# Optimization experiments

Hardware: AMD Instinct MI355X
Metric: run time of the kernel (lower is better)

Reference implementation:

```python
import jax, jax.numpy as jnp
import numpy as np

B, N, D = 16, 1024, 1152
H = 16; DH = D // H
GH = GW = 32; SY = SX = 2
WS = SY * SX                      # tokens per window
NW = (GH // SY) * (GW // SX)      # 256 windows (one dst each)
NS = NW * (WS - 1)                # 768 src tokens
NUM_PRUNE = int(N * 0.5)          # 512
NOISE_ALPHA = 0.1
SIM_BETA = 1.0


def setup_inputs() -> dict:
    key = jax.random.key(0)
    ks = jax.random.split(key, 8)
    rn = lambda k, s: jax.random.normal(k, s, jnp.float32) * 0.02
    return dict(
        x=jax.random.normal(ks[0], (B, N, D), jnp.float32),
        noise=jax.random.uniform(ks[1], (B, NW, WS), jnp.float32),
        ln1_g=jnp.ones((D,), jnp.float32), ln1_b=jnp.zeros((D,), jnp.float32),
        ln2_g=jnp.ones((D,), jnp.float32), ln2_b=jnp.zeros((D,), jnp.float32),
        w_qkv=rn(ks[2], (D, 3 * D)), b_qkv=jnp.zeros((3 * D,), jnp.float32),
        w_proj=rn(ks[3], (D, D)), b_proj=jnp.zeros((D,), jnp.float32),
        w_fc1=rn(ks[4], (D, 4 * D)), b_fc1=jnp.zeros((4 * D,), jnp.float32),
        w_fc2=rn(ks[5], (4 * D, D)), b_fc2=jnp.zeros((D,), jnp.float32),
    )


def _ln(x, g, b):
    mu = x.mean(-1, keepdims=True)
    var = ((x - mu) ** 2).mean(-1, keepdims=True)
    return (x - mu) * jax.lax.rsqrt(var + 1e-6) * g + b


def _dit_block(x, ln1_g, ln1_b, ln2_g, ln2_b, w_qkv, b_qkv, w_proj, b_proj,
               w_fc1, b_fc1, w_fc2, b_fc2):
    Bq, T, _ = x.shape
    y = _ln(x, ln1_g, ln1_b)
    q, k, v = jnp.split(y @ w_qkv + b_qkv, 3, axis=-1)
    hd = lambda t: t.reshape(Bq, T, H, DH).transpose(0, 2, 1, 3)  # [B,H,T,DH]
    q, k, v = hd(q), hd(k), hd(v)
    att = jax.nn.softmax(jnp.einsum('bhqd,bhkd->bhqk', q, k) * (1.0 / np.sqrt(DH)), axis=-1)
    o = jnp.einsum('bhqk,bhkd->bhqd', att, v).transpose(0, 2, 1, 3).reshape(Bq, T, D)
    x = x + o @ w_proj + b_proj
    y = _ln(x, ln2_g, ln2_b)
    return x + jax.nn.gelu(y @ w_fc1 + b_fc1) @ w_fc2 + b_fc2


def _sito_indices(x, noise):
    # SiTo seed (dst) selection + similarity-based prune index computation.
    xn = x / (jnp.linalg.norm(x, axis=-1, keepdims=True) + 1e-6)  # cosine feats
    grid = jnp.arange(N).reshape(GH, GW)
    win = grid.reshape(GH // SY, SY, GW // SX, SX).transpose(0, 2, 1, 3).reshape(NW, WS)
    xw = xn[:, win]                                   # [B,NW,WS,D]
    mean = xw.mean(2, keepdims=True)
    score = SIM_BETA * (xw * mean).sum(-1) + NOISE_ALPHA * noise  # [B,NW,WS]
    dst_local = jnp.argmax(score, axis=-1)            # [B,NW]
    winb = jnp.broadcast_to(win, (B, NW, WS))
    dst_idx = jnp.take_along_axis(winb, dst_local[..., None], -1)[..., 0]  # [B,NW]
    local = jnp.arange(WS)[None, None]
    keymat = jnp.where(local != dst_local[..., None], local, WS)
    src_local = jnp.sort(keymat, -1)[..., : WS - 1]   # non-dst locals, in order
    src_idx = jnp.take_along_axis(winb, src_local, -1).reshape(B, NS)
    a = jnp.take_along_axis(xn, src_idx[..., None], 1)      # [B,NS,D]
    bf = jnp.take_along_axis(xn, dst_idx[..., None], 1)     # [B,NW,D]
    sim = jnp.einsum('bsd,bnd->bsn', a, bf)                 # [B,NS,NW]
    best = jnp.argmax(sim, -1)                              # most-similar dst
    order = jnp.argsort(-jnp.max(sim, -1), axis=-1)
    pruned_pos = order[:, :NUM_PRUNE]
    kept_pos = order[:, NUM_PRUNE:]
    src_kept = jnp.take_along_axis(src_idx, kept_pos, 1)
    src_pruned = jnp.take_along_axis(src_idx, pruned_pos, 1)
    pruned_best = jnp.take_along_axis(best, pruned_pos, 1)
    return dst_idx, src_kept, src_pruned, pruned_best


def reference(x, noise, ln1_g, ln1_b, ln2_g, ln2_b, w_qkv, b_qkv, w_proj, b_proj,
              w_fc1, b_fc1, w_fc2, b_fc2):
    dst_idx, src_kept, src_pruned, pruned_best = _sito_indices(x, noise)
    keep_idx = jnp.concatenate([dst_idx, src_kept], axis=1)          # [B,Nk]
    xk = jnp.take_along_axis(x, keep_idx[..., None], 1)              # prune_fn
    out = _dit_block(xk, ln1_g, ln1_b, ln2_g, ln2_b, w_qkv, b_qkv,
                     w_proj, b_proj, w_fc1, b_fc1, w_fc2, b_fc2)

    def recover_one(o, di, sk, sp, pb):  # recover_fn: scatter + copy-from-dst
        out_dst, out_src = o[:NW], o[NW:]
        full = jnp.zeros((N, D), o.dtype)
        full = full.at[di].set(out_dst)
        full = full.at[sk].set(out_src)
        return full.at[sp].set(out_dst[pb])

    return jax.vmap(recover_one)(out, dst_idx, src_kept, src_pruned, pruned_best)
```

## Files before the change

kernel.cpp:

```cpp
#include <hip/hip_runtime.h>
#include <hip/hip_bf16.h>

namespace {

constexpr int Dd = 1152;

typedef __attribute__((ext_vector_type(8))) short bf16x8;
typedef __attribute__((ext_vector_type(4))) float f32x4;

__device__ __forceinline__ void gload_lds16(const void* g, void* l) {
  __builtin_amdgcn_global_load_lds(
      (const __attribute__((address_space(1))) void*)g,
      (__attribute__((address_space(3))) void*)l, 16, 0, 0);
}

__device__ __forceinline__ float gelu_f(float x) {
  float x3 = x * x * x;
  float z2 = 1.5957691216057308f * (x + 0.044715f * x3);
  float e = __expf(fminf(z2, 30.0f));
  return x * e / (e + 1.0f);
}

__global__ __launch_bounds__(256) void normwin_kernel(const float* __restrict__ x,
    const float* __restrict__ noise, float* __restrict__ inv,
    __hip_bfloat16* __restrict__ xnh, __hip_bfloat16* __restrict__ xnl,
    int* __restrict__ dsti, int* __restrict__ srci) {
  const int gidx = blockIdx.x;
  const int b = gidx >> 8, w = gidx & 255;
  const int wy = w >> 4, wx = w & 15;
  const int t0 = wy * 64 + wx * 2;
  const int wid = threadIdx.x >> 6, lane = threadIdx.x & 63;
  const int tok = t0 + (wid >> 1) * 32 + (wid & 1);
  const int row = (b << 10) + tok;

  const float2* xr = (const float2*)(x + (size_t)row * Dd);
  float2 v[9];
  float s = 0.f;
  #pragma unroll
  for (int e = 0; e < 9; ++e) {
    v[e] = xr[lane + 64 * e];
    s += v[e].x * v[e].x + v[e].y * v[e].y;
  }
  #pragma unroll
  for (int m = 1; m < 64; m <<= 1) s += __shfl_xor(s, m);
  float iv = 1.0f / (sqrtf(s) + 1e-6f);
  if (lane == 0) inv[row] = iv;

  __shared__ float2 xns[4][576];
  ushort2* ph = (ushort2*)(xnh + (size_t)row * Dd);
  ushort2* pl = (ushort2*)(xnl + (size_t)row * Dd);
  #pragma unroll
  for (int e = 0; e < 9; ++e) {
    float ax = v[e].x * iv, ay = v[e].y * iv;
    xns[wid][lane + 64 * e] = make_float2(ax, ay);
    __hip_bfloat16 hx = __float2bfloat16(ax), hy = __float2bfloat16(ay);
    __hip_bfloat16 lx = __float2bfloat16(ax - __bfloat162float(hx));
    __hip_bfloat16 ly = __float2bfloat16(ay - __bfloat162float(hy));
    ph[lane + 64 * e] = make_ushort2(*(ushort*)&hx, *(ushort*)&hy);
    pl[lane + 64 * e] = make_ushort2(*(ushort*)&lx, *(ushort*)&ly);
  }
  __syncthreads();

  float dot = 0.f;
  #pragma unroll
  for (int e = 0; e < 9; ++e) {
    int i = lane + 64 * e;
    float2 a0 = xns[0][i], a1 = xns[1][i], a2 = xns[2][i], a3 = xns[3][i];
    float sx = a0.x + a1.x + a2.x + a3.x;
    float sy = a0.y + a1.y + a2.y + a3.y;
    dot += (v[e].x * iv) * sx + (v[e].y * iv) * sy;
  }
  #pragma unroll
  for (int m = 1; m < 64; m <<= 1) dot += __shfl_xor(dot, m);
  __shared__ float dots[4];
  if (lane == 0) dots[wid] = dot;
  __syncthreads();
  if (threadIdx.x == 0) {
    float best = -1e30f; int bj = 0;
    #pragma unroll
    for (int j = 0; j < 4; ++j) {
      float sc = 0.25f * dots[j] + 0.1f * noise[(size_t)gidx * 4 + j];
      if (sc > best) { best = sc; bj = j; }
    }
    int tk[4] = {t0, t0 + 1, t0 + 32, t0 + 33};
    dsti[b * 256 + w] = tk[bj];
    int m = 0;
    #pragma unroll
    for (int j = 0; j < 4; ++j) if (j != bj) srci[b * 768 + w * 3 + (m++)] = tk[j];
  }
}

__global__ __launch_bounds__(256) void simgemm_kernel(
    const __hip_bfloat16* __restrict__ xnh, const __hip_bfloat16* __restrict__ xnl,
    const int* __restrict__ dsti, const int* __restrict__ srci,
    float* __restrict__ mx, int* __restrict__ best) {
  int b = blockIdx.x / 12;
  int m0 = (blockIdx.x % 12) * 64;
  __shared__ __align__(16) __hip_bfloat16 AsH[2][64 * 32];
  __shared__ __align__(16) __hip_bfloat16 AsL[2][64 * 32];
  __shared__ __align__(16) __hip_bfloat16 BsH[2][256 * 32];
  __shared__ __align__(16) __hip_bfloat16 BsL[2][256 * 32];
  const int tid = threadIdx.x, wid = tid >> 6, lane = tid & 63;
  const int g = lane >> 4, lr = lane & 15;

  const int slotRow = tid >> 2;
  const int colByte = (((tid & 3) ^ ((tid >> 3) & 3)) << 4);
  size_t aRow = (size_t)((b << 10) + srci[b * 768 + m0 + slotRow]) * Dd;
  size_t bRow[4];
  #pragma unroll
  for (int p = 0; p < 4; ++p)
    bRow[p] = (size_t)((b << 10) + dsti[b * 256 + p * 64 + slotRow]) * Dd;
  const char* xh = (const char*)xnh;
  const char* xl = (const char*)xnl;

  auto stage = [&](int buf, int k0) {
    size_t ka = (aRow + k0) * 2 + colByte;
    gload_lds16(xh + ka, (char*)AsH + buf * 4096 + wid * 1024);
    gload_lds16(xl + ka, (char*)AsL + buf * 4096 + wid * 1024);
    #pragma unroll
    for (int p = 0; p < 4; ++p) {
      size_t kb = (bRow[p] + k0) * 2 + colByte;
      gload_lds16(xh + kb, (char*)BsH + buf * 16384 + p * 4096 + wid * 1024);
      gload_lds16(xl + kb, (char*)BsL + buf * 16384 + p * 4096 + wid * 1024);
    }
  };

  f32x4 hh[16], hx[16];
  const f32x4 zf = {0.f, 0.f, 0.f, 0.f};
  #pragma unroll
  for (int nf = 0; nf < 16; ++nf) { hh[nf] = zf; hx[nf] = zf; }

  const int roff = ((g ^ ((lr >> 1) & 3)) << 3);
  stage(0, 0);
  asm volatile("s_waitcnt vmcnt(0)" ::: "memory");
  __syncthreads();
  int buf = 0;
  for (int ks = 0; ks < 36; ++ks) {
    if (ks + 1 < 36) stage(buf ^ 1, (ks + 1) * 32);
    bf16x8 ah = *(const bf16x8*)&AsH[buf][(wid * 16 + lr) * 32 + roff];
    bf16x8 al = *(const bf16x8*)&AsL[buf][(wid * 16 + lr) * 32 + roff];
    #pragma unroll
    for (int nf = 0; nf < 16; ++nf) {
      bf16x8 bh = *(const bf16x8*)&BsH[buf][(nf * 16 + lr) * 32 + roff];
      bf16x8 bl = *(const bf16x8*)&BsL[buf][(nf * 16 + lr) * 32 + roff];
      hh[nf] = __builtin_amdgcn_mfma_f32_16x16x32_bf16(ah, bh, hh[nf], 0, 0, 0);
      hx[nf] = __builtin_amdgcn_mfma_f32_16x16x32_bf16(ah, bl, hx[nf], 0, 0, 0);
      hx[nf] = __builtin_amdgcn_mfma_f32_16x16x32_bf16(al, bh, hx[nf], 0, 0, 0);
    }
    asm volatile("s_waitcnt vmcnt(0)" ::: "memory");
    __syncthreads();
    buf ^= 1;
  }

  #pragma unroll
  for (int j = 0; j < 4; ++j) {
    float bv = -1e30f; int bi = 0;
    #pragma unroll
    for (int nf = 0; nf < 16; ++nf) {
      float v = hh[nf][j] + hx[nf][j];
      if (v > bv) { bv = v; bi = nf * 16 + lr; }
    }
    #pragma unroll
    for (int m = 1; m < 16; m <<= 1) {
      float ov = __shfl_xor(bv, m);
      int oi = __shfl_xor(bi, m);
      if (ov > bv || (ov == bv && oi < bi)) { bv = ov; bi = oi; }
    }
    if (lr == 0) {
      int row = m0 + wid * 16 + g * 4 + j;
      mx[b * 768 + row] = bv;
      best[b * 768 + row] = bi;
    }
  }
}

__global__ __launch_bounds__(256) void rank_kernel(const float* __restrict__ mx,
    const int* __restrict__ best, const int* __restrict__ dsti,
    const int* __restrict__ srci, int* __restrict__ keep, int* __restrict__ srow) {
  int b = blockIdx.x;
  int tid = threadIdx.x;
  __shared__ float smx[768];
  for (int i = tid; i < 768; i += 256) smx[i] = mx[b * 768 + i];
  __syncthreads();
  if (tid < 256) {
    int t = dsti[b * 256 + tid];
    keep[b * 512 + tid] = t;
    srow[b * 1024 + t] = tid;
  }
  for (int i = tid; i < 768; i += 256) {
    float v = smx[i];
    int r = 0;
    for (int s = 0; s < 768; ++s) {
      float u = smx[s];
      r += (u > v) || (u == v && s < i);
    }
    int tok = srci[b * 768 + i];
    if (r >= 512) {
      keep[b * 512 + (r - 256)] = tok;
      srow[b * 1024 + tok] = r - 256;
    } else {
      srow[b * 1024 + tok] = best[b * 768 + i];
    }
  }
}

template<int GATHER>
__global__ __launch_bounds__(256) void ln_kernel(const float* __restrict__ xin,
    const int* __restrict__ keep, const float* __restrict__ gw,
    const float* __restrict__ bw, __hip_bfloat16* __restrict__ yout) {
  int row = blockIdx.x;
  const float* xr;
  if (GATHER) {
    int b = row >> 9, t = row & 511;
    int tok = keep[(b << 9) + t];
    xr = xin + (size_t)((b << 10) + tok) * Dd;
  } else {
    xr = xin + (size_t)row * Dd;
  }
  int tid = threadIdx.x;
  float v[5];
  float s = 0.f, s2 = 0.f;
  #pragma unroll
  for (int e = 0; e < 5; ++e) {
    int i = tid + e * 256;
    float val = (i < Dd) ? xr[i] : 0.f;
    v[e] = val; s += val; s2 += val * val;
  }
  #pragma unroll
  for (int m = 1; m < 64; m <<= 1) { s += __shfl_xor(s, m); s2 += __shfl_xor(s2, m); }
  __shared__ float ps[4], ps2[4];
  int wid = tid >> 6, lane = tid & 63;
  if (lane == 0) { ps[wid] = s; ps2[wid] = s2; }
  __syncthreads();
  s = ps[0] + ps[1] + ps[2] + ps[3];
  s2 = ps2[0] + ps2[1] + ps2[2] + ps2[3];
  constexpr float inv_d = 1.0f / Dd;
  float mu = s * inv_d;
  float var = s2 * inv_d - mu * mu;
  float rstd = rsqrtf(var + 1e-6f);
  __hip_bfloat16* yr = yout + (size_t)row * Dd;
  #pragma unroll
  for (int e = 0; e < 5; ++e) {
    int i = tid + e * 256;
    if (i < Dd) {
      yr[i] = __float2bfloat16((v[e] - mu) * rstd * gw[i] + bw[i]);
    }
  }
}

__global__ __launch_bounds__(256) void wtrans_kernel(const float* __restrict__ w,
    __hip_bfloat16* __restrict__ wT, int K, int N) {
  __shared__ float tile[32][33];
  int nt = N >> 5;
  int tk = blockIdx.x / nt, tn = blockIdx.x % nt;
  int tid = threadIdx.x;
  #pragma unroll
  for (int e = 0; e < 4; ++e) {
    int idx = tid + e * 256;
    int r = idx >> 5, c = idx & 31;
    tile[r][c] = w[(size_t)(tk * 32 + r) * N + tn * 32 + c];
  }
  __syncthreads();
  #pragma unroll
  for (int e = 0; e < 4; ++e) {
    int idx = tid + e * 256;
    int r = idx >> 5, c = idx & 31;
    wT[(size_t)(tn * 32 + r) * K + tk * 32 + c] = __float2bfloat16(tile[c][r]);
  }
}

template<int EPI>
__device__ __forceinline__ void epi_store(void* C, const float* res, int Nd,
                                          size_t row, size_t col, float v) {
  if (EPI == 0) {
    ((__hip_bfloat16*)C)[row * (size_t)Nd + col] = __float2bfloat16(v);
  } else if (EPI == 1) {
    ((float*)C)[row * (size_t)Nd + col] = v + res[row * (size_t)Nd + col];
  } else if (EPI == 2) {
    ((__hip_bfloat16*)C)[row * (size_t)Nd + col] = __float2bfloat16(gelu_f(v));
  }
}

template<int EPI>
__global__ __launch_bounds__(512, 4) void gemm128_kernel(
    const __hip_bfloat16* __restrict__ A, const __hip_bfloat16* __restrict__ BT,
    const float* __restrict__ bias, const float* __restrict__ res,
    const int* __restrict__ keepIdx, const float* __restrict__ xsrc,
    void* __restrict__ C, int Md, int Nd, int NdPad, int Kd) {
  constexpr int BM = 128;
  __shared__ __align__(16) __hip_bfloat16 As[3][BM * 32];
  __shared__ __align__(16) __hip_bfloat16 Bs[3][256 * 32];
  const int nb = NdPad >> 8;
  const int q8 = gridDim.x >> 3;
  const int wg = (blockIdx.x & 7) * q8 + (blockIdx.x >> 3);
  const int bm = wg / nb, bnb = wg % nb;
  const int tid = threadIdx.x, wid = tid >> 6, lane = tid & 63;
  const int g = lane >> 4, lr = lane & 15;
  const int wm = wid >> 2, wn = wid & 3;
  const size_t m0 = (size_t)bm * BM, n0 = (size_t)bnb * 256;

  const int trow = tid >> 2;
  const int scol = (((tid & 3) ^ ((tid >> 3) & 3)) << 3);
  const char* Ab = (const char*)A;
  const char* Bb = (const char*)BT;

  auto stage = [&](int slot, int kt) {
    const size_t kb = ((size_t)kt << 5) + scol;
    gload_lds16(Ab + (((m0 + trow) * (size_t)Kd + kb) << 1),
                (char*)As + slot * 8192 + wid * 1024);
    gload_lds16(Bb + (((n0 + trow) * (size_t)Kd + kb) << 1),
                (char*)Bs + slot * 16384 + wid * 1024);
    gload_lds16(Bb + (((n0 + 128 + trow) * (size_t)Kd + kb) << 1),
                (char*)Bs + slot * 16384 + 8192 + wid * 1024);
  };

  f32x4 acc[4][4];
  const f32x4 zf = {0.f, 0.f, 0.f, 0.f};
  #pragma unroll
  for (int mi = 0; mi < 4; ++mi)
    #pragma unroll
    for (int ni = 0; ni < 4; ++ni) acc[mi][ni] = zf;

  const int nk = Kd >> 5;
  stage(0, 0);
  stage(1, 1);
  asm volatile("s_waitcnt vmcnt(3)" ::: "memory");
  __builtin_amdgcn_s_barrier();

  int cur = 0;
  const int roff = ((g ^ ((lr >> 1) & 3)) << 3);
  for (int kt = 0; kt < nk; ++kt) {
    const __hip_bfloat16* Ac = As[cur];
    const __hip_bfloat16* Bc = Bs[cur];
    bf16x8 af[4], bf[4];
    #pragma unroll
    for (int mi = 0; mi < 4; ++mi)
      af[mi] = *(const bf16x8*)&Ac[(wm * 64 + mi * 16 + lr) * 32 + roff];
    #pragma unroll
    for (int ni = 0; ni < 4; ++ni)
      bf[ni] = *(const bf16x8*)&Bc[(wn * 64 + ni * 16 + lr) * 32 + roff];
    if (kt + 2 < nk) stage(cur == 0 ? 2 : cur - 1, kt + 2);
    __builtin_amdgcn_s_barrier();
    __builtin_amdgcn_s_setprio(1);
    #pragma unroll
    for (int mi = 0; mi < 4; ++mi)
      #pragma unroll
      for (int ni = 0; ni < 4; ++ni)
        acc[mi][ni] = __builtin_amdgcn_mfma_f32_16x16x32_bf16(af[mi], bf[ni], acc[mi][ni], 0, 0, 0);
    __builtin_amdgcn_s_setprio(0);
    if (kt + 2 < nk)      asm volatile("s_waitcnt vmcnt(3)" ::: "memory");
    else if (kt + 1 < nk) asm volatile("s_waitcnt vmcnt(0)" ::: "memory");
    __builtin_amdgcn_s_barrier();
    cur = (cur == 2) ? 0 : cur + 1;
  }

  #pragma unroll
  for (int ni = 0; ni < 4; ++ni) {
    size_t col = n0 + wn * 64 + ni * 16 + lr;
    if (col < (size_t)Nd) {
      float bv = bias[col];
      #pragma unroll
      for (int mi = 0; mi < 4; ++mi) {
        #pragma unroll
        for (int j = 0; j < 4; ++j) {
          size_t row = m0 + wm * 64 + mi * 16 + g * 4 + j;
          float v = acc[mi][ni][j] + bv;
          if (EPI == 3) {
            int b = (int)(row >> 9);
            int tok = keepIdx[row];
            const float* rr = xsrc + ((size_t)(b << 10) + tok) * Dd;
            ((float*)C)[row * (size_t)Nd + col] = v + rr[col];
          } else {
            epi_store<EPI>(C, res, Nd, row, col, v);
          }
        }
      }
    }
  }
}

template<int EPI>
__global__ __launch_bounds__(256, 3) void gemm128n_kernel(
    const __hip_bfloat16* __restrict__ A, const __hip_bfloat16* __restrict__ BT,
    const float* __restrict__ bias, const float* __restrict__ res,
    const int* __restrict__ keepIdx, const float* __restrict__ xsrc,
    void* __restrict__ C, int Md, int Nd, int Kd) {
  __shared__ __align__(16) __hip_bfloat16 As[3][128 * 32];
  __shared__ __align__(16) __hip_bfloat16 Bs[3][128 * 32];
  const int nb = Nd >> 7;
  const int q8 = gridDim.x >> 3;
  const int wg = (blockIdx.x & 7) * q8 + (blockIdx.x >> 3);
  const int bm = wg / nb, bnb = wg % nb;
  const int tid = threadIdx.x, wid = tid >> 6, lane = tid & 63;
  const int g = lane >> 4, lr = lane & 15;
  const int wm = wid >> 1, wn = wid & 1;
  const size_t m0 = (size_t)bm * 128, n0 = (size_t)bnb * 128;

  const int trow = tid >> 2;
  const int scol = (((tid & 3) ^ ((tid >> 3) & 3)) << 3);
  const char* Ab = (const char*)A;
  const char* Bb = (const char*)BT;

  auto stage = [&](int slot, int kt) {
    const size_t kb = ((size_t)kt << 5) + scol;
    #pragma unroll
    for (int c = 0; c < 2; ++c)
      gload_lds16(Ab + (((m0 + c * 64 + trow) * (size_t)Kd + kb) << 1),
                  (char*)As + slot * 8192 + c * 4096 + tid * 16);
    #pragma unroll
    for (int c = 0; c < 2; ++c)
      gload_lds16(Bb + (((n0 + c * 64 + trow) * (size_t)Kd + kb) << 1),
                  (char*)Bs + slot * 8192 + c * 4096 + tid * 16);
  };

  f32x4 acc[4][4];
  const f32x4 zf = {0.f, 0.f, 0.f, 0.f};
  #pragma unroll
  for (int mi = 0; mi < 4; ++mi)
    #pragma unroll
    for (int ni = 0; ni < 4; ++ni) acc[mi][ni] = zf;

  const int nk = Kd >> 5;
  stage(0, 0);
  stage(1, 1);
  asm volatile("s_waitcnt vmcnt(4)" ::: "memory");
  __builtin_amdgcn_s_barrier();

  int cur = 0;
  const int roff = ((g ^ ((lr >> 1) & 3)) << 3);
  for (int kt = 0; kt < nk; ++kt) {
    const __hip_bfloat16* Ac = As[cur];
    const __hip_bfloat16* Bc = Bs[cur];
    bf16x8 af[4], bf[4];
    #pragma unroll
    for (int mi = 0; mi < 4; ++mi)
      af[mi] = *(const bf16x8*)&Ac[(wm * 64 + mi * 16 + lr) * 32 + roff];
    #pragma unroll
    for (int ni = 0; ni < 4; ++ni)
      bf[ni] = *(const bf16x8*)&Bc[(wn * 64 + ni * 16 + lr) * 32 + roff];
    if (kt + 2 < nk) stage(cur == 0 ? 2 : cur - 1, kt + 2);
    __builtin_amdgcn_s_barrier();
    __builtin_amdgcn_s_setprio(1);
    #pragma unroll
    for (int mi = 0; mi < 4; ++mi)
      #pragma unroll
      for (int ni = 0; ni < 4; ++ni)
        acc[mi][ni] = __builtin_amdgcn_mfma_f32_16x16x32_bf16(af[mi], bf[ni], acc[mi][ni], 0, 0, 0);
    __builtin_amdgcn_s_setprio(0);
    if (kt + 2 < nk)      asm volatile("s_waitcnt vmcnt(4)" ::: "memory");
    else if (kt + 1 < nk) asm volatile("s_waitcnt vmcnt(0)" ::: "memory");
    __builtin_amdgcn_s_barrier();
    cur = (cur == 2) ? 0 : cur + 1;
  }

  #pragma unroll
  for (int ni = 0; ni < 4; ++ni) {
    size_t col = n0 + wn * 64 + ni * 16 + lr;
    float bv = bias[col];
    #pragma unroll
    for (int mi = 0; mi < 4; ++mi) {
      #pragma unroll
      for (int j = 0; j < 4; ++j) {
        size_t row = m0 + wm * 64 + mi * 16 + g * 4 + j;
        float v = acc[mi][ni][j] + bv;
        if (EPI == 3) {
          int b = (int)(row >> 9);
          int tok = keepIdx[row];
          const float* rr = xsrc + ((size_t)(b << 10) + tok) * Dd;
          ((float*)C)[row * (size_t)Nd + col] = v + rr[col];
        } else {
          epi_store<EPI>(C, res, Nd, row, col, v);
        }
      }
    }
  }
}

__global__ __launch_bounds__(256) void vtrans_kernel(const __hip_bfloat16* __restrict__ qkv,
                                                     __hip_bfloat16* __restrict__ vT) {
  int bh = blockIdx.x;
  int b = bh >> 4, h = bh & 15;
  __shared__ __align__(16) __hip_bfloat16 Vl[256 * 72];
  int tid = threadIdx.x;
  const __hip_bfloat16 zb = __float2bfloat16(0.0f);
  for (int half = 0; half < 2; ++half) {
    __syncthreads();
    for (int idx = tid; idx < 256 * 18; idx += 256) {
      int t = idx / 18, c = idx % 18;
      *(ushort4*)&Vl[t * 72 + c * 4] =
          *(const ushort4*)&qkv[((size_t)(b * 512 + half * 256 + t)) * 3456 + 2304 + h * 72 + c * 4];
    }
    __syncthreads();
    for (int idx = tid; idx < 80 * 256; idx += 256) {
      int d = idx >> 8, t = idx & 255;
      vT[((size_t)bh * 80 + d) * 512 + half * 256 + t] = (d < 72) ? Vl[t * 72 + d] : zb;
    }
  }
}

__global__ __launch_bounds__(256) void attn_kernel(const __hip_bfloat16* __restrict__ qkv,
    const __hip_bfloat16* __restrict__ vT, __hip_bfloat16* __restrict__ o) {
  const int blk = blockIdx.x;
  const int qt = blk & 7, bh = blk >> 3;
  const int b = bh >> 4, h = bh & 15;
  __shared__ __align__(16) __hip_bfloat16 Qs[64][96];
  __shared__ __align__(16) __hip_bfloat16 Ks[64][96];
  __shared__ __align__(16) __hip_bfloat16 Vs[80][72];
  __shared__ __align__(16) __hip_bfloat16 Ps[4][16][72];
  const int tid = threadIdx.x, wid = tid >> 6, lane = tid & 63;
  const int g = lane >> 4, lr = lane & 15;
  const __hip_bfloat16 zb = __float2bfloat16(0.0f);

  for (int idx = tid; idx < 64 * 18; idx += 256) {
    int r = idx / 18, c = idx % 18;
    *(ushort4*)&Qs[r][c * 4] =
        *(const ushort4*)&qkv[((size_t)(b * 512 + qt * 64 + r)) * 3456 + h * 72 + c * 4];
  }
  for (int idx = tid; idx < 64 * 24; idx += 256) {
    int r = idx / 24, d = 72 + idx % 24;
    Qs[r][d] = zb; Ks[r][d] = zb;
  }

  f32x4 ov[5];
  const f32x4 zf = {0.f, 0.f, 0.f, 0.f};
  #pragma unroll
  for (int ni = 0; ni < 5; ++ni) ov[ni] = zf;
  float m_[4], l_[4];
  #pragma unroll
  for (int j = 0; j < 4; ++j) { m_[j] = -3.0e38f; l_[j] = 0.f; }
  const float scale = 0.11785113019775793f;

  for (int c = 0; c < 8; ++c) {
    __syncthreads();
    for (int idx = tid; idx < 64 * 18; idx += 256) {
      int r = idx / 18, cc = idx % 18;
      *(ushort4*)&Ks[r][cc * 4] =
          *(const ushort4*)&qkv[((size_t)(b * 512 + c * 64 + r)) * 3456 + 1152 + h * 72 + cc * 4];
    }
    for (int idx = tid; idx < 80 * 8; idx += 256) {
      int d = idx >> 3, t8 = idx & 7;
      *(uint4*)&Vs[d][t8 * 8] =
          *(const uint4*)&vT[((size_t)bh * 80 + d) * 512 + c * 64 + t8 * 8];
    }
    __syncthreads();

    f32x4 sf[4];
    #pragma unroll
    for (int nf = 0; nf < 4; ++nf) sf[nf] = zf;
    #pragma unroll
    for (int ks = 0; ks < 3; ++ks) {
      bf16x8 qa = *(const bf16x8*)&Qs[wid * 16 + lr][ks * 32 + g * 8];
      #pragma unroll
      for (int nf = 0; nf < 4; ++nf) {
        bf16x8 kb = *(const bf16x8*)&Ks[nf * 16 + lr][ks * 32 + g * 8];
        sf[nf] = __builtin_amdgcn_mfma_f32_16x16x32_bf16(qa, kb, sf[nf], 0, 0, 0);
      }
    }

    float cm[4];
    #pragma unroll
    for (int j = 0; j < 4; ++j)
      cm[j] = fmaxf(fmaxf(sf[0][j], sf[1][j]), fmaxf(sf[2][j], sf[3][j])) * scale;
    #pragma unroll
    for (int mm = 1; mm < 16; mm <<= 1)
      #pragma unroll
      for (int j = 0; j < 4; ++j) cm[j] = fmaxf(cm[j], __shfl_xor(cm[j], mm));
    float fac[4], rs[4];
    #pragma unroll
    for (int j = 0; j < 4; ++j) {
      float nm = fmaxf(m_[j], cm[j]);
      fac[j] = __expf(m_[j] - nm);
      m_[j] = nm;
      rs[j] = 0.f;
    }
    #pragma unroll
    for (int nf = 0; nf < 4; ++nf)
      #pragma unroll
      for (int j = 0; j < 4; ++j) {
        float pv = __expf(sf[nf][j] * scale - m_[j]);
        rs[j] += pv;
        Ps[wid][g * 4 + j][nf * 16 + lr] = __float2bfloat16(pv);
      }
    #pragma unroll
    for (int mm = 1; mm < 16; mm <<= 1)
      #pragma unroll
      for (int j = 0; j < 4; ++j) rs[j] += __shfl_xor(rs[j], mm);
    #pragma unroll
    for (int j = 0; j < 4; ++j) l_[j] = l_[j] * fac[j] + rs[j];
    #pragma unroll
    for (int ni = 0; ni < 5; ++ni)
      #pragma unroll
      for (int j = 0; j < 4; ++j) ov[ni][j] *= fac[j];

    #pragma unroll
    for (int k2 = 0; k2 < 2; ++k2) {
      bf16x8 pa = *(const bf16x8*)&Ps[wid][lr][k2 * 32 + g * 8];
      #pragma unroll
      for (int ni = 0; ni < 5; ++ni) {
        bf16x8 vb = *(const bf16x8*)&Vs[ni * 16 + lr][k2 * 32 + g * 8];
        ov[ni] = __builtin_amdgcn_mfma_f32_16x16x32_bf16(pa, vb, ov[ni], 0, 0, 0);
      }
    }
  }

  #pragma unroll
  for (int ni = 0; ni < 5; ++ni) {
    int d = ni * 16 + lr;
    if (d < 72) {
      #pragma unroll
      for (int j = 0; j < 4; ++j) {
        int t = qt * 64 + wid * 16 + g * 4 + j;
        o[((size_t)(b * 512 + t)) * 1152 + h * 72 + d] = __float2bfloat16(ov[ni][j] / l_[j]);
      }
    }
  }
}

__global__ __launch_bounds__(256) void recover_kernel(const float* __restrict__ yout,
    const int* __restrict__ srow, float* __restrict__ out) {
  int idx = blockIdx.x * 256 + threadIdx.x;
  int q = idx % 288;
  int bnv = idx / 288;
  int r = srow[bnv];
  int b = bnv >> 10;
  const float4* src = (const float4*)yout + ((size_t)((b << 9) + r)) * 288 + q;
  ((float4*)out)[idx] = *src;
}

}

extern "C" void kernel_launch(void* const* d_in, const int* in_sizes, int n_in,
                              void* d_out, int out_size, void* d_ws, size_t ws_size,
                              hipStream_t stream) {
  (void)in_sizes; (void)n_in; (void)out_size; (void)ws_size;
  const float* x      = (const float*)d_in[0];
  const float* noise  = (const float*)d_in[1];
  const float* ln1_g  = (const float*)d_in[2];
  const float* ln1_b  = (const float*)d_in[3];
  const float* ln2_g  = (const float*)d_in[4];
  const float* ln2_b  = (const float*)d_in[5];
  const float* w_qkv  = (const float*)d_in[6];
  const float* b_qkv  = (const float*)d_in[7];
  const float* w_proj = (const float*)d_in[8];
  const float* b_proj = (const float*)d_in[9];
  const float* w_fc1  = (const float*)d_in[10];
  const float* b_fc1  = (const float*)d_in[11];
  const float* w_fc2  = (const float*)d_in[12];
  const float* b_fc2  = (const float*)d_in[13];
  float* out = (float*)d_out;

  char* p = (char*)d_ws;
  auto alloc = [&](size_t bytes) {
    char* r = p;
    p += (bytes + 255) & ~(size_t)255;
    return r;
  };
  __hip_bfloat16* wqkvT  = (__hip_bfloat16*)alloc((size_t)3584 * 1152 * 2);
  __hip_bfloat16* wprojT = (__hip_bfloat16*)alloc((size_t)1280 * 1152 * 2);
  __hip_bfloat16* wfc1T  = (__hip_bfloat16*)alloc((size_t)4608 * 1152 * 2);
  __hip_bfloat16* wfc2T  = (__hip_bfloat16*)alloc((size_t)1280 * 4608 * 2);
  float* inv = (float*)alloc(16384 * 4);
  int* dsti  = (int*)alloc(4096 * 4);
  int* srci  = (int*)alloc(12288 * 4);
  float* mx  = (float*)alloc(12288 * 4);
  int* best  = (int*)alloc(12288 * 4);
  int* keep  = (int*)alloc(8192 * 4);
  int* srow  = (int*)alloc(16384 * 4);
  float* yout = (float*)alloc((size_t)8192 * 1152 * 4);
  __hip_bfloat16* y1   = (__hip_bfloat16*)alloc((size_t)8192 * 1152 * 2);
  __hip_bfloat16* qkvb = (__hip_bfloat16*)alloc((size_t)8192 * 4608 * 2);
  __hip_bfloat16* vT   = (__hip_bfloat16*)alloc((size_t)256 * 80 * 512 * 2);
  __hip_bfloat16* ob   = (__hip_bfloat16*)alloc((size_t)8192 * 1152 * 2);
  float* x2 = (float*)alloc((size_t)8192 * 1152 * 4);

  __hip_bfloat16* xnh = qkvb;
  __hip_bfloat16* xnl = qkvb + (size_t)16 * 1024 * 1152;

  wtrans_kernel<<<36 * 108, 256, 0, stream>>>(w_qkv, wqkvT, 1152, 3456);
  wtrans_kernel<<<36 * 36, 256, 0, stream>>>(w_proj, wprojT, 1152, 1152);
  wtrans_kernel<<<36 * 144, 256, 0, stream>>>(w_fc1, wfc1T, 1152, 4608);
  wtrans_kernel<<<144 * 36, 256, 0, stream>>>(w_fc2, wfc2T, 4608, 1152);

  normwin_kernel<<<4096, 256, 0, stream>>>(x, noise, inv, xnh, xnl, dsti, srci);
  simgemm_kernel<<<16 * 12, 256, 0, stream>>>(xnh, xnl, dsti, srci, mx, best);
  rank_kernel<<<16, 256, 0, stream>>>(mx, best, dsti, srci, keep, srow);

  ln_kernel<1><<<8192, 256, 0, stream>>>(x, keep, ln1_g, ln1_b, y1);
  gemm128_kernel<0><<<64 * 14, 512, 0, stream>>>(y1, wqkvT, b_qkv, nullptr, nullptr, nullptr,
                                                 qkvb, 8192, 3456, 3584, 1152);
  vtrans_kernel<<<256, 256, 0, stream>>>(qkvb, vT);
  attn_kernel<<<2048, 256, 0, stream>>>(qkvb, vT, ob);
  gemm128n_kernel<3><<<64 * 9, 256, 0, stream>>>(ob, wprojT, b_proj, nullptr, keep, x,
                                                 x2, 8192, 1152, 1152);
  ln_kernel<0><<<8192, 256, 0, stream>>>(x2, nullptr, ln2_g, ln2_b, y1);
  gemm128n_kernel<2><<<64 * 36, 256, 0, stream>>>(y1, wfc1T, b_fc1, nullptr, nullptr, nullptr,
                                                  qkvb, 8192, 4608, 1152);
  gemm128n_kernel<1><<<64 * 9, 256, 0, stream>>>(qkvb, wfc2T, b_fc2, x2, nullptr, nullptr,
                                                 yout, 8192, 1152, 4608);

  recover_kernel<<<18432, 256, 0, stream>>>(yout, srow, out);
}
```

Measured before the change: 735.7 us.

## Double-buffer LDS fragment reads and deepen prefetch in 128x128 GEMM mainloop

Restructures the 128x128 GEMM main loop to prefetch three K-tiles up front and to register-double-buffer the LDS fragment reads, loading the next tile's fragments before issuing the current tile's MFMAs. This cuts the loop to one barrier per K step instead of two and lets LDS reads overlap with matrix math. The cost is more live registers for the second fragment set, which could pressure occupancy at the launch bounds of 3 waves. Unused EPI==3 code is also dropped from the gemm128_kernel epilogue.

```diff
diff --git a/kernel.cpp b/kernel.cpp
--- a/kernel.cpp
+++ b/kernel.cpp
@@ -365,14 +365,7 @@
         for (int j = 0; j < 4; ++j) {
           size_t row = m0 + wm * 64 + mi * 16 + g * 4 + j;
           float v = acc[mi][ni][j] + bv;
-          if (EPI == 3) {
-            int b = (int)(row >> 9);
-            int tok = keepIdx[row];
-            const float* rr = xsrc + ((size_t)(b << 10) + tok) * Dd;
-            ((float*)C)[row * (size_t)Nd + col] = v + rr[col];
-          } else {
-            epi_store<EPI>(C, res, Nd, row, col, v);
-          }
+          epi_store<EPI>(C, res, Nd, row, col, v);
         }
       }
     }
@@ -380,7 +373,7 @@
 }
 
 template<int EPI>
-__global__ __launch_bounds__(256, 3) void gemm128n_kernel(
+__global__ __launch_bounds__(256, 3) void gemm128v_kernel(
     const __hip_bfloat16* __restrict__ A, const __hip_bfloat16* __restrict__ BT,
     const float* __restrict__ bias, const float* __restrict__ res,
     const int* __restrict__ keepIdx, const float* __restrict__ xsrc,
@@ -420,38 +413,52 @@
     #pragma unroll
     for (int ni = 0; ni < 4; ++ni) acc[mi][ni] = zf;
 
+  const int roff = ((g ^ ((lr >> 1) & 3)) << 3);
   const int nk = Kd >> 5;
-  stage(0, 0);
-  stage(1, 1);
-  asm volatile("s_waitcnt vmcnt(4)" ::: "memory");
+
+  bf16x8 afA[4], bfA[4], afB[4], bfB[4];
+
+#define DSREAD(AF, BF, SLOT) { \
+  const __hip_bfloat16* Ac_ = As[SLOT]; \
+  const __hip_bfloat16* Bc_ = Bs[SLOT]; \
+  _Pragma("unroll") for (int mi_ = 0; mi_ < 4; ++mi_) \
+    AF[mi_] = *(const bf16x8*)&Ac_[(wm * 64 + mi_ * 16 + lr) * 32 + roff]; \
+  _Pragma("unroll") for (int ni_ = 0; ni_ < 4; ++ni_) \
+    BF[ni_] = *(const bf16x8*)&Bc_[(wn * 64 + ni_ * 16 + lr) * 32 + roff]; }
+
+#define MFMA16(AF, BF) { \
+  __builtin_amdgcn_s_setprio(1); \
+  _Pragma("unroll") for (int mi_ = 0; mi_ < 4; ++mi_) \
+    _Pragma("unroll") for (int ni_ = 0; ni_ < 4; ++ni_) \
+      acc[mi_][ni_] = __builtin_amdgcn_mfma_f32_16x16x32_bf16(AF[mi_], BF[ni_], acc[mi_][ni_], 0, 0, 0); \
+  __builtin_amdgcn_s_setprio(0); }
+
+#define GITER(KT, S0, S1, AFC, BFC, AFN, BFN) { \
+  if ((KT) <= nk - 3)      { asm volatile("s_waitcnt vmcnt(4)" ::: "memory"); } \
+  else if ((KT) == nk - 2) { asm volatile("s_waitcnt vmcnt(0)" ::: "memory"); } \
+  asm volatile("s_waitcnt lgkmcnt(0)" ::: "memory"); \
+  __builtin_amdgcn_s_barrier(); \
+  asm volatile("" ::: "memory"); \
+  if ((KT) + 1 < nk) DSREAD(AFN, BFN, (S1)); \
+  if ((KT) + 3 < nk) stage((S0), (KT) + 3); \
+  MFMA16(AFC, BFC); }
+
+  stage(0, 0); stage(1, 1); stage(2, 2);
+  asm volatile("s_waitcnt vmcnt(8)" ::: "memory");
   __builtin_amdgcn_s_barrier();
-
-  int cur = 0;
-  const int roff = ((g ^ ((lr >> 1) & 3)) << 3);
-  for (int kt = 0; kt < nk; ++kt) {
-    const __hip_bfloat16* Ac = As[cur];
-    const __hip_bfloat16* Bc = Bs[cur];
-    bf16x8 af[4], bf[4];
-    #pragma unroll
-    for (int mi = 0; mi < 4; ++mi)
-      af[mi] = *(const bf16x8*)&Ac[(wm * 64 + mi * 16 + lr) * 32 + roff];
-    #pragma unroll
-    for (int ni = 0; ni < 4; ++ni)
-      bf[ni] = *(const bf16x8*)&Bc[(wn * 64 + ni * 16 + lr) * 32 + roff];
-    if (kt + 2 < nk) stage(cur == 0 ? 2 : cur - 1, kt + 2);
-    __builtin_amdgcn_s_barrier();
-    __builtin_amdgcn_s_setprio(1);
-    #pragma unroll
-    for (int mi = 0; mi < 4; ++mi)
-      #pragma unroll
-      for (int ni = 0; ni < 4; ++ni)
-        acc[mi][ni] = __builtin_amdgcn_mfma_f32_16x16x32_bf16(af[mi], bf[ni], acc[mi][ni], 0, 0, 0);
-    __builtin_amdgcn_s_setprio(0);
-    if (kt + 2 < nk)      asm volatile("s_waitcnt vmcnt(4)" ::: "memory");
-    else if (kt + 1 < nk) asm volatile("s_waitcnt vmcnt(0)" ::: "memory");
-    __builtin_amdgcn_s_barrier();
-    cur = (cur == 2) ? 0 : cur + 1;
-  }
+  asm volatile("" ::: "memory");
+  DSREAD(afA, bfA, 0);
+
+  int s0 = 0, s1 = 1;
+  for (int kt = 0; kt < nk; kt += 2) {
+    GITER(kt, s0, s1, afA, bfA, afB, bfB);
+    int s2 = (s1 == 2) ? 0 : s1 + 1;
+    GITER(kt + 1, s1, s2, afB, bfB, afA, bfA);
+    s0 = s2; s1 = (s2 == 2) ? 0 : s2 + 1;
+  }
+#undef GITER
+#undef MFMA16
+#undef DSREAD
 
   #pragma unroll
   for (int ni = 0; ni < 4; ++ni) {
@@ -690,12 +697,12 @@
                                                  qkvb, 8192, 3456, 3584, 1152);
   vtrans_kernel<<<256, 256, 0, stream>>>(qkvb, vT);
   attn_kernel<<<2048, 256, 0, stream>>>(qkvb, vT, ob);
-  gemm128n_kernel<3><<<64 * 9, 256, 0, stream>>>(ob, wprojT, b_proj, nullptr, keep, x,
+  gemm128v_kernel<3><<<64 * 9, 256, 0, stream>>>(ob, wprojT, b_proj, nullptr, keep, x,
                                                  x2, 8192, 1152, 1152);
   ln_kernel<0><<<8192, 256, 0, stream>>>(x2, nullptr, ln2_g, ln2_b, y1);
-  gemm128n_kernel<2><<<64 * 36, 256, 0, stream>>>(y1, wfc1T, b_fc1, nullptr, nullptr, nullptr,
+  gemm128v_kernel<2><<<64 * 36, 256, 0, stream>>>(y1, wfc1T, b_fc1, nullptr, nullptr, nullptr,
                                                   qkvb, 8192, 4608, 1152);
-  gemm128n_kernel<1><<<64 * 9, 256, 0, stream>>>(qkvb, wfc2T, b_fc2, x2, nullptr, nullptr,
+  gemm128v_kernel<1><<<64 * 9, 256, 0, stream>>>(qkvb, wfc2T, b_fc2, x2, nullptr, nullptr,
                                                  yout, 8192, 1152, 4608);
 
   recover_kernel<<<18432, 256, 0, stream>>>(yout, srow, out);
```

Result: no change. 734.6 us (-0.1%).
